# Optimization experiments

Hardware: AMD Instinct MI355X
Metric: run time of the kernel (lower is better)

The kernel has to match this reference:

```python
import math
import jax, jax.numpy as jnp
import numpy as np

HEADS = 8


def setup_inputs() -> dict:
    key = jax.random.key(0)
    ks = jax.random.split(key, 8)
    B, L, S, C = 2, 1024, 2048, 1280
    CORR = 256  # native seg_corr resolution; nearest-upsampled x4 to (1024, 1024)
    sc = 0.02
    return {
        "hidden_states": jax.random.normal(ks[0], (B, L, C), jnp.float32),
        "encoder_hidden_states": jax.random.normal(ks[1], (B, S, C), jnp.float32),
        "seg_corr": jax.random.randint(ks[2], (B, CORR, CORR), 0, 2, jnp.int32),
        "Wq": jax.random.normal(ks[3], (C, C), jnp.float32) * sc,
        "Wk": jax.random.normal(ks[4], (C, C), jnp.float32) * sc,
        "Wv": jax.random.normal(ks[5], (C, C), jnp.float32) * sc,
        "Wo": jax.random.normal(ks[6], (C, C), jnp.float32) * sc,
        "bo": jnp.zeros((C,), jnp.float32),
    }


def reference(hidden_states, encoder_hidden_states, seg_corr, Wq, Wk, Wv, Wo, bo):
    B, L, C = hidden_states.shape
    S = encoder_hidden_states.shape[1]
    H = HEADS
    d = C // H

    # projections -> [B, H, L, d] / [B, H, S, d]
    q = (hidden_states @ Wq).reshape(B, L, H, d).transpose(0, 2, 1, 3)
    k = (encoder_hidden_states @ Wk).reshape(B, S, H, d).transpose(0, 2, 1, 3)
    v = (encoder_hidden_states @ Wv).reshape(B, S, H, d).transpose(0, 2, 1, 3)

    scale = 1.0 / math.sqrt(d)
    scores = jnp.einsum("bhld,bhsd->bhls", q, k) * scale  # [B, H, L, S]

    half = S // 2  # S == 2L in the match-attention branch
    # nearest-neighbor upsample of seg_corr to (L, half) == integer repeat
    rL = L // seg_corr.shape[1]
    rS = half // seg_corr.shape[2]
    corr = jnp.repeat(jnp.repeat(seg_corr, rL, axis=1), rS, axis=2)[:, None]  # [B,1,L,half]

    # hard correlation mask on the second half of keys (reference-image tokens)
    masked = jnp.where(corr == 1, scores[..., half:], jnp.float32(-jnp.inf))
    scores = jnp.concatenate([scores[..., :half], masked], axis=-1)

    attn_weight = jax.nn.softmax(scores, axis=-1)  # dropout_p = 0.0
    out = jnp.einsum("bhls,bhsd->bhld", attn_weight, v)
    out = out.transpose(0, 2, 1, 3).reshape(B, L, C)

    out = out @ Wo + bo            # to_out[0]; to_out[1] dropout is identity at p=0
    out = out + hidden_states      # residual connection; rescale_output_factor = 1
    return out
```

## Files before the change

kernel.cpp:

```cpp
#include <hip/hip_runtime.h>

typedef unsigned short u16;
typedef unsigned int   u32;
typedef unsigned char  u8;

using bf16x8 = __attribute__((ext_vector_type(8))) __bf16;
using f32x4  = __attribute__((ext_vector_type(4))) float;
using s16x4  = __attribute__((ext_vector_type(4))) short;

__device__ __forceinline__ u16 f2bf(float f) {
    u32 u = __float_as_uint(f);
    return (u16)((u + 0x7FFFu + ((u >> 16) & 1u)) >> 16);
}

#define MFMA(a, b, c) __builtin_amdgcn_mfma_f32_16x16x32_bf16((a), (b), (c), 0, 0, 0)
#define MFMA16(a, b, c) __builtin_amdgcn_mfma_f32_16x16x16bf16_1k((a), (b), (c), 0, 0, 0)

__device__ __forceinline__ void gll16(const u16* g, u16* l) {
    __builtin_amdgcn_global_load_lds(
        (const __attribute__((address_space(1))) void*)g,
        (__attribute__((address_space(3))) void*)l, 16, 0, 0);
}

__global__ __launch_bounds__(256) void wtrans_kernel(
    const float* __restrict__ W0, const float* __restrict__ W1,
    const float* __restrict__ W2, const float* __restrict__ W3,
    u16* __restrict__ T0, u16* __restrict__ T1,
    u16* __restrict__ T2, u16* __restrict__ T3) {
    const int N = 1280;
    const int z = blockIdx.z;
    const float* W = (z == 0) ? W0 : (z == 1) ? W1 : (z == 2) ? W2 : W3;
    u16* T = (z == 0) ? T0 : (z == 1) ? T1 : (z == 2) ? T2 : T3;
    __shared__ float t[32][33];
    const int bx = blockIdx.x * 32, by = blockIdx.y * 32;
    const int x = threadIdx.x, ty = threadIdx.y;
#pragma unroll
    for (int j = 0; j < 4; j++) {
        const int y = ty + j * 8;
        t[y][x] = W[(size_t)(by + y) * N + (bx + x)];
    }
    __syncthreads();
#pragma unroll
    for (int j = 0; j < 4; j++) {
        const int y = ty + j * 8;
        T[(size_t)(bx + y) * N + (by + x)] = f2bf(t[x][y]);
    }
}

__global__ __launch_bounds__(256) void conv_kernel(const float* __restrict__ in,
                                                   u16* __restrict__ out, int n8) {
    const int i = blockIdx.x * 256 + threadIdx.x;
    if (i >= n8) return;
    const float4 a = ((const float4*)in)[i * 2];
    const float4 b = ((const float4*)in)[i * 2 + 1];
    union { uint4 u; u16 s[8]; } cv;
    cv.s[0] = f2bf(a.x); cv.s[1] = f2bf(a.y); cv.s[2] = f2bf(a.z); cv.s[3] = f2bf(a.w);
    cv.s[4] = f2bf(b.x); cv.s[5] = f2bf(b.y); cv.s[6] = f2bf(b.z); cv.s[7] = f2bf(b.w);
    ((uint4*)out)[i] = cv.u;
}

template <int MI, bool TRANSC, bool EPI>
__global__ __launch_bounds__(256) void gemm2_kernel(
    const u16* __restrict__ A, const u16* __restrict__ Bt, void* __restrict__ Cp,
    const float* __restrict__ bias, const float* __restrict__ resid,
    const int M, const int N, const int K) {
    __shared__ __align__(16) u16 Al[2][MI * 32 * 64];
    __shared__ __align__(16) u16 Bl[2][128 * 64];
    const int tid = threadIdx.x;
    const int lane = tid & 63, w = tid >> 6;
    const int wr = w >> 1, wc = w & 1;
    const int lr = lane & 15, lq = lane >> 4;
    const int m0 = blockIdx.y * (MI * 32), n0 = blockIdx.x * 128;

    const int f_r = tid >> 3;
    const int srcch = (tid & 7) ^ ((tid >> 3) & 7);
    const int ldst = (tid & 192) * 8;

    const f32x4 fzero = {0.f, 0.f, 0.f, 0.f};
    f32x4 acc[MI][4];
#pragma unroll
    for (int i = 0; i < MI; i++)
#pragma unroll
        for (int j = 0; j < 4; j++) acc[i][j] = fzero;

    const int nkt = K >> 6;

#define STAGE(buf, kt)                                                          \
    {                                                                           \
        const int k0s = (kt) << 6;                                              \
        _Pragma("unroll")                                                       \
        for (int i = 0; i < MI; i++) {                                          \
            const int r = i * 32 + f_r;                                         \
            gll16(&A[(size_t)(m0 + r) * K + k0s + srcch * 8],                   \
                  &Al[buf][i * 2048 + ldst]);                                   \
        }                                                                       \
        _Pragma("unroll")                                                       \
        for (int i = 0; i < 4; i++) {                                           \
            const int r = i * 32 + f_r;                                         \
            gll16(&Bt[(size_t)(n0 + r) * K + k0s + srcch * 8],                  \
                  &Bl[buf][i * 2048 + ldst]);                                   \
        }                                                                       \
    }

    STAGE(0, 0);
    asm volatile("s_waitcnt vmcnt(0)" ::: "memory");
    __syncthreads();
    int cur = 0;
    for (int kt = 0; kt < nkt; kt++) {
        if (kt + 1 < nkt) STAGE(cur ^ 1, kt + 1);
#pragma unroll
        for (int ks = 0; ks < 2; ks++) {
            bf16x8 af[MI], bfv[4];
#pragma unroll
            for (int mi = 0; mi < MI; mi++) {
                const int rowA = wr * (MI * 16) + mi * 16 + lr;
                af[mi] = *(const bf16x8*)&Al[cur][rowA * 64 +
                                                  (((ks * 4 + lq) ^ (rowA & 7)) << 3)];
            }
#pragma unroll
            for (int ni = 0; ni < 4; ni++) {
                const int rowB = wc * 64 + ni * 16 + lr;
                bfv[ni] = *(const bf16x8*)&Bl[cur][rowB * 64 +
                                                   (((ks * 4 + lq) ^ (rowB & 7)) << 3)];
            }
#pragma unroll
            for (int mi = 0; mi < MI; mi++)
#pragma unroll
                for (int ni = 0; ni < 4; ni++)
                    acc[mi][ni] = MFMA(af[mi], bfv[ni], acc[mi][ni]);
        }
        asm volatile("s_waitcnt vmcnt(0)" ::: "memory");
        __syncthreads();
        cur ^= 1;
    }
#undef STAGE

#pragma unroll
    for (int mi = 0; mi < MI; mi++)
#pragma unroll
        for (int ni = 0; ni < 4; ni++)
#pragma unroll
            for (int j = 0; j < 4; j++) {
                const int row = m0 + wr * (MI * 16) + mi * 16 + lq * 4 + j;
                const int col = n0 + wc * 64 + ni * 16 + lr;
                const float v = acc[mi][ni][j];
                if (EPI) {
                    ((float*)Cp)[(size_t)row * N + col] =
                        v + bias[col] + resid[(size_t)row * N + col];
                } else if (TRANSC) {
                    ((u16*)Cp)[((size_t)(col >> 11) * 1280 + row) * 2048 +
                               (col & 2047)] = f2bf(v);
                } else {
                    ((u16*)Cp)[(size_t)row * N + col] = f2bf(v);
                }
            }
}

__global__ __launch_bounds__(256) void attn_kernel(
    const u16* __restrict__ qb, const u16* __restrict__ kb,
    const u16* __restrict__ vtb, const int* __restrict__ seg,
    u16* __restrict__ ao) {
    __shared__ __align__(16) u16 arena[20224];
    const int KL = 0;
    const int VT = 10752;
    const int PT = 17152;
    const int SG = 18944;
    const int ML = 19968;
    u8* segl8 = (u8*)&arena[SG];
    float* Mlf = (float*)&arena[ML];
    float* Osum = (float*)&arena[KL];

    const int tid = threadIdx.x;
    const int lane = tid & 63, w = tid >> 6;
    const int qg = w >> 1, kc = w & 1;
    const int lr = lane & 15, lq = lane >> 4;
    const int id = blockIdx.x;
    const int h = id & 7, bz = (id >> 3) & 1, qt = id >> 4;

#pragma unroll
    for (int i = 0; i < 2; i++) {
        const int4 v =
            *(const int4*)&seg[(size_t)(bz * 256 + qt * 8) * 256 + tid * 8 + i * 4];
        segl8[tid * 8 + i * 4 + 0] = (u8)v.x;
        segl8[tid * 8 + i * 4 + 1] = (u8)v.y;
        segl8[tid * 8 + i * 4 + 2] = (u8)v.z;
        segl8[tid * 8 + i * 4 + 3] = (u8)v.w;
    }

    bf16x8 qf[5];
    {
        const size_t qrow =
            (size_t)(bz * 1024 + qt * 32 + qg * 16 + lr) * 1280 + h * 160;
#pragma unroll
        for (int ks = 0; ks < 5; ks++)
            qf[ks] = *(const bf16x8*)&qb[qrow + ks * 32 + lq * 8];
    }

    const int nk0 = tid, nk1 = tid + 256;
    const int nv0 = tid, nv1 = tid + 256;
    const bool exK = (tid < 128);
    const int ne = exK ? (512 + tid) : (512 + tid - 128);
    const int gok0 = (nk0 / 20) * 1280 + (nk0 % 20) * 8;
    const int lok0 = (nk0 / 20) * 168 + (nk0 % 20) * 8;
    const int gok1 = (nk1 / 20) * 1280 + (nk1 % 20) * 8;
    const int lok1 = (nk1 / 20) * 168 + (nk1 % 20) * 8;
    const int gov0 = (nv0 >> 2) * 2048 + (nv0 & 3) * 8;
    const int lov0 = (nv0 >> 2) * 40 + (nv0 & 3) * 8;
    const int gov1 = (nv1 >> 2) * 2048 + (nv1 & 3) * 8;
    const int lov1 = (nv1 >> 2) * 40 + (nv1 & 3) * 8;
    const int goe = exK ? ((ne / 20) * 1280 + (ne % 20) * 8)
                        : ((ne >> 2) * 2048 + (ne & 3) * 8);
    const int loe = exK ? ((ne / 20) * 168 + (ne % 20) * 8)
                        : ((ne >> 2) * 40 + (ne & 3) * 8);

    const u16* kT = kb + (size_t)(bz * 2048) * 1280 + h * 160;
    const u16* vT = vtb + (size_t)(bz * 1280 + h * 160) * 2048;

    const f32x4 fzero = {0.f, 0.f, 0.f, 0.f};
    f32x4 oacc[10];
#pragma unroll
    for (int d = 0; d < 10; d++) oacc[d] = fzero;
    f32x4 oaccL = fzero;
    float m_i[4] = {0.f, 0.f, 0.f, 0.f};
    const float sc = 0.07905694150420949f;
    const s16x4 ones = {(short)0x3F80, (short)0x3F80, (short)0x3F80, (short)0x3F80};
    u16* ptw = &arena[PT + w * 448];

    uint4 rk0 = *(const uint4*)&kT[gok0];
    uint4 rk1 = *(const uint4*)&kT[gok1];
    uint4 rv0 = *(const uint4*)&vT[gov0];
    uint4 rv1 = *(const uint4*)&vT[gov1];
    uint4 re  = exK ? *(const uint4*)&kT[goe] : *(const uint4*)&vT[goe];

    for (int kt = 0; kt < 64; kt++) {
        __syncthreads();
        *(uint4*)&arena[KL + lok0] = rk0;
        *(uint4*)&arena[KL + lok1] = rk1;
        *(uint4*)&arena[VT + lov0] = rv0;
        *(uint4*)&arena[VT + lov1] = rv1;
        if (exK) *(uint4*)&arena[KL + loe] = re;
        else     *(uint4*)&arena[VT + loe] = re;
        if (kt + 1 < 64) {
            const u16* kTn = kT + (size_t)(kt + 1) * 40960;
            const u16* vTn = vT + (kt + 1) * 32;
            rk0 = *(const uint4*)&kTn[gok0];
            rk1 = *(const uint4*)&kTn[gok1];
            rv0 = *(const uint4*)&vTn[gov0];
            rv1 = *(const uint4*)&vTn[gov1];
            re  = exK ? *(const uint4*)&kTn[goe] : *(const uint4*)&vTn[goe];
        }
        __syncthreads();

        f32x4 s4 = fzero;
#pragma unroll
        for (int ks = 0; ks < 5; ks++) {
            const bf16x8 bk =
                *(const bf16x8*)&arena[KL + (kc * 16 + lr) * 168 + ks * 32 + lq * 8];
            s4 = MFMA(qf[ks], bk, s4);
        }
        float msk = 0.f;
        if (kt >= 32) {
            const int sg = (kt - 32) * 8 + kc * 4 + (lr >> 2);
            msk = segl8[(qg * 4 + lq) * 256 + sg] ? 0.f : -1e30f;
        }
#pragma unroll
        for (int j = 0; j < 4; j++) s4[j] = s4[j] * sc + msk;

        const bool ex = (s4[0] > m_i[0] + 8.f) || (s4[1] > m_i[1] + 8.f) ||
                        (s4[2] > m_i[2] + 8.f) || (s4[3] > m_i[3] + 8.f);
        if (__any(ex)) {
#pragma unroll
            for (int j = 0; j < 4; j++) {
                float rm = s4[j];
                rm = fmaxf(rm, __shfl_xor(rm, 1));
                rm = fmaxf(rm, __shfl_xor(rm, 2));
                rm = fmaxf(rm, __shfl_xor(rm, 4));
                rm = fmaxf(rm, __shfl_xor(rm, 8));
                const float mn = fmaxf(m_i[j], rm);
                const float al = __expf(m_i[j] - mn);
#pragma unroll
                for (int d = 0; d < 10; d++) oacc[d][j] *= al;
                oaccL[j] *= al;
                m_i[j] = mn;
            }
        }
#pragma unroll
        for (int j = 0; j < 4; j++) {
            const float e = __expf(s4[j] - m_i[j]);
            ptw[(lq * 4 + j) * 28 + lr] = f2bf(e);
        }
        const s16x4 pa = *(const s16x4*)&ptw[lr * 28 + lq * 4];
        oaccL = MFMA16(pa, ones, oaccL);
#pragma unroll
        for (int nt2 = 0; nt2 < 10; nt2++) {
            const s16x4 bv =
                *(const s16x4*)&arena[VT + (nt2 * 16 + lr) * 40 + kc * 16 + lq * 4];
            oacc[nt2] = MFMA16(pa, bv, oacc[nt2]);
        }
    }

    if (lr == 0) {
#pragma unroll
        for (int j = 0; j < 4; j++) {
            Mlf[(w * 16 + lq * 4 + j) * 2 + 0] = m_i[j];
            Mlf[(w * 16 + lq * 4 + j) * 2 + 1] = oaccL[j];
        }
    }
    __syncthreads();
    float aj[4], inv[4];
#pragma unroll
    for (int j = 0; j < 4; j++) {
        const int row = lq * 4 + j;
        const float m1 = Mlf[((w ^ 1) * 16 + row) * 2];
        const float l1 = Mlf[((w ^ 1) * 16 + row) * 2 + 1];
        const float M = fmaxf(m_i[j], m1);
        aj[j] = __expf(m_i[j] - M);
        inv[j] = 1.f / (oaccL[j] * aj[j] + l1 * __expf(m1 - M));
    }
    if (kc == 1) {
#pragma unroll
        for (int nt2 = 0; nt2 < 10; nt2++)
#pragma unroll
            for (int j = 0; j < 4; j++)
                Osum[(qg * 16 + lq * 4 + j) * 164 + nt2 * 16 + lr] =
                    oacc[nt2][j] * aj[j];
    }
    __syncthreads();
    if (kc == 0) {
#pragma unroll
        for (int nt2 = 0; nt2 < 10; nt2++)
#pragma unroll
            for (int j = 0; j < 4; j++) {
                const int row = lq * 4 + j;
                const float v = (oacc[nt2][j] * aj[j] +
                                 Osum[(qg * 16 + row) * 164 + nt2 * 16 + lr]) *
                                inv[j];
                ao[(size_t)(bz * 1024 + qt * 32 + qg * 16 + row) * 1280 + h * 160 +
                   nt2 * 16 + lr] = f2bf(v);
            }
    }
}

extern "C" void kernel_launch(void* const* d_in, const int* in_sizes, int n_in,
                              void* d_out, int out_size, void* d_ws, size_t ws_size,
                              hipStream_t stream) {
    const float* hs  = (const float*)d_in[0];
    const float* ehs = (const float*)d_in[1];
    const int*   seg = (const int*)d_in[2];
    const float* Wq  = (const float*)d_in[3];
    const float* Wk  = (const float*)d_in[4];
    const float* Wv  = (const float*)d_in[5];
    const float* Wo  = (const float*)d_in[6];
    const float* bo  = (const float*)d_in[7];
    float* out = (float*)d_out;

    u16* base  = (u16*)d_ws;
    u16* WoT   = base;
    u16* qbuf  = WoT + 1638400;
    u16* kbuf  = qbuf + 2621440;
    u16* vtbuf = kbuf + 5242880;
    u16* hbuf  = vtbuf + 5242880;
    u16* ebuf  = hbuf + 2621440;
    u16* WqT   = ebuf + 5242880;
    u16* WkT   = WqT + 1638400;
    u16* WvT   = WkT + 1638400;
    u16* aobuf = hbuf;

    dim3 tb(32, 8), tg(40, 40, 4);
    wtrans_kernel<<<tg, tb, 0, stream>>>(Wq, Wk, Wv, Wo, WqT, WkT, WvT, WoT);
    conv_kernel<<<1280, 256, 0, stream>>>(hs, hbuf, 327680);
    conv_kernel<<<2560, 256, 0, stream>>>(ehs, ebuf, 655360);

    gemm2_kernel<2, false, false><<<dim3(10, 32), 256, 0, stream>>>(
        hbuf, WqT, qbuf, nullptr, nullptr, 2048, 1280, 1280);
    gemm2_kernel<4, false, false><<<dim3(10, 32), 256, 0, stream>>>(
        ebuf, WkT, kbuf, nullptr, nullptr, 4096, 1280, 1280);
    gemm2_kernel<4, true, false><<<dim3(32, 10), 256, 0, stream>>>(
        WvT, ebuf, vtbuf, nullptr, nullptr, 1280, 4096, 1280);

    attn_kernel<<<512, 256, 0, stream>>>(qbuf, kbuf, vtbuf, seg, aobuf);

    gemm2_kernel<2, false, true><<<dim3(10, 32), 256, 0, stream>>>(
        aobuf, WoT, out, bo, hs, 2048, 1280, 1280);
}
```

Baseline: 190.8 us.

## Double attention key tile, use 16x16x32 MFMA for PV, shrink GEMM tiles

The attention kernel now processes 64 keys per iteration instead of 32, halving loop trips and barriers. Each wave computes two 16-key score tiles and uses the wider 16x16x32 bf16 MFMA for both P·V and the row-sum, with K/V staged through more LDS per iteration. Separately, the projection GEMMs switch to smaller M tiles, doubling grid size so more CUs stay busy, and the two fp32-to-bf16 conversion launches merge into one. The larger LDS footprint and register use may reduce attention occupancy, and the smaller GEMM tiles reduce data reuse per block.

```diff
diff --git a/kernel.cpp b/kernel.cpp
--- a/kernel.cpp
+++ b/kernel.cpp
@@ -6,7 +6,6 @@
 
 using bf16x8 = __attribute__((ext_vector_type(8))) __bf16;
 using f32x4  = __attribute__((ext_vector_type(4))) float;
-using s16x4  = __attribute__((ext_vector_type(4))) short;
 
 __device__ __forceinline__ u16 f2bf(float f) {
     u32 u = __float_as_uint(f);
@@ -14,7 +13,6 @@
 }
 
 #define MFMA(a, b, c) __builtin_amdgcn_mfma_f32_16x16x32_bf16((a), (b), (c), 0, 0, 0)
-#define MFMA16(a, b, c) __builtin_amdgcn_mfma_f32_16x16x16bf16_1k((a), (b), (c), 0, 0, 0)
 
 __device__ __forceinline__ void gll16(const u16* g, u16* l) {
     __builtin_amdgcn_global_load_lds(
@@ -47,10 +45,14 @@
     }
 }
 
-__global__ __launch_bounds__(256) void conv_kernel(const float* __restrict__ in,
-                                                   u16* __restrict__ out, int n8) {
-    const int i = blockIdx.x * 256 + threadIdx.x;
-    if (i >= n8) return;
+__global__ __launch_bounds__(256) void conv2_kernel(const float* __restrict__ in0,
+                                                    u16* __restrict__ out0,
+                                                    const float* __restrict__ in1,
+                                                    u16* __restrict__ out1) {
+    const int bid = blockIdx.x;
+    const float* in = (bid < 1280) ? in0 : in1;
+    u16* out = (bid < 1280) ? out0 : out1;
+    const int i = ((bid < 1280) ? bid : bid - 1280) * 256 + threadIdx.x;
     const float4 a = ((const float4*)in)[i * 2];
     const float4 b = ((const float4*)in)[i * 2 + 1];
     union { uint4 u; u16 s[8]; } cv;
@@ -160,12 +162,12 @@
     const u16* __restrict__ qb, const u16* __restrict__ kb,
     const u16* __restrict__ vtb, const int* __restrict__ seg,
     u16* __restrict__ ao) {
-    __shared__ __align__(16) u16 arena[20224];
+    __shared__ __align__(16) u16 arena[26112];
     const int KL = 0;
     const int VT = 10752;
-    const int PT = 17152;
-    const int SG = 18944;
-    const int ML = 19968;
+    const int PT = 22272;
+    const int SG = 24832;
+    const int ML = 25856;
     u8* segl8 = (u8*)&arena[SG];
     float* Mlf = (float*)&arena[ML];
     float* Osum = (float*)&arena[KL];
@@ -196,25 +198,20 @@
             qf[ks] = *(const bf16x8*)&qb[qrow + ks * 32 + lq * 8];
     }
 
-    const int nk0 = tid, nk1 = tid + 256;
-    const int nv0 = tid, nv1 = tid + 256;
-    const bool exK = (tid < 128);
-    const int ne = exK ? (512 + tid) : (512 + tid - 128);
-    const int gok0 = (nk0 / 20) * 1280 + (nk0 % 20) * 8;
-    const int lok0 = (nk0 / 20) * 168 + (nk0 % 20) * 8;
-    const int gok1 = (nk1 / 20) * 1280 + (nk1 % 20) * 8;
-    const int lok1 = (nk1 / 20) * 168 + (nk1 % 20) * 8;
-    const int gov0 = (nv0 >> 2) * 2048 + (nv0 & 3) * 8;
-    const int lov0 = (nv0 >> 2) * 40 + (nv0 & 3) * 8;
-    const int gov1 = (nv1 >> 2) * 2048 + (nv1 & 3) * 8;
-    const int lov1 = (nv1 >> 2) * 40 + (nv1 & 3) * 8;
-    const int goe = exK ? ((ne / 20) * 1280 + (ne % 20) * 8)
-                        : ((ne >> 2) * 2048 + (ne & 3) * 8);
-    const int loe = exK ? ((ne / 20) * 168 + (ne % 20) * 8)
-                        : ((ne >> 2) * 40 + (ne & 3) * 8);
-
-    const u16* kT = kb + (size_t)(bz * 2048) * 1280 + h * 160;
-    const u16* vT = vtb + (size_t)(bz * 1280 + h * 160) * 2048;
+    int gok[5], lok[5], gov[5], lov[5];
+#pragma unroll
+    for (int i = 0; i < 5; i++) {
+        const int n = i * 256 + tid;
+        const int kr = n / 20, kcol = n % 20;
+        gok[i] = kr * 1280 + kcol * 8;
+        lok[i] = kr * 168 + kcol * 8;
+        const int d = n >> 3, vc = n & 7;
+        gov[i] = d * 2048 + vc * 8;
+        lov[i] = d * 72 + vc * 8;
+    }
+
+    const u16* kP = kb + (size_t)(bz * 2048) * 1280 + h * 160;
+    const u16* vP = vtb + (size_t)(bz * 1280 + h * 160) * 2048;
 
     const f32x4 fzero = {0.f, 0.f, 0.f, 0.f};
     f32x4 oacc[10];
@@ -223,55 +220,69 @@
     f32x4 oaccL = fzero;
     float m_i[4] = {0.f, 0.f, 0.f, 0.f};
     const float sc = 0.07905694150420949f;
-    const s16x4 ones = {(short)0x3F80, (short)0x3F80, (short)0x3F80, (short)0x3F80};
-    u16* ptw = &arena[PT + w * 448];
-
-    uint4 rk0 = *(const uint4*)&kT[gok0];
-    uint4 rk1 = *(const uint4*)&kT[gok1];
-    uint4 rv0 = *(const uint4*)&vT[gov0];
-    uint4 rv1 = *(const uint4*)&vT[gov1];
-    uint4 re  = exK ? *(const uint4*)&kT[goe] : *(const uint4*)&vT[goe];
-
-    for (int kt = 0; kt < 64; kt++) {
+    bf16x8 ones8;
+#pragma unroll
+    for (int e = 0; e < 8; e++) {
+        const u16 one = 0x3F80;
+        ones8[e] = *(const __bf16*)&one;
+    }
+    u16* ptw = &arena[PT + w * 640];
+
+    uint4 rk[5], rv[5];
+#pragma unroll
+    for (int i = 0; i < 5; i++) {
+        rk[i] = *(const uint4*)&kP[gok[i]];
+        rv[i] = *(const uint4*)&vP[gov[i]];
+    }
+
+    for (int kt = 0; kt < 32; kt++) {
         __syncthreads();
-        *(uint4*)&arena[KL + lok0] = rk0;
-        *(uint4*)&arena[KL + lok1] = rk1;
-        *(uint4*)&arena[VT + lov0] = rv0;
-        *(uint4*)&arena[VT + lov1] = rv1;
-        if (exK) *(uint4*)&arena[KL + loe] = re;
-        else     *(uint4*)&arena[VT + loe] = re;
-        if (kt + 1 < 64) {
-            const u16* kTn = kT + (size_t)(kt + 1) * 40960;
-            const u16* vTn = vT + (kt + 1) * 32;
-            rk0 = *(const uint4*)&kTn[gok0];
-            rk1 = *(const uint4*)&kTn[gok1];
-            rv0 = *(const uint4*)&vTn[gov0];
-            rv1 = *(const uint4*)&vTn[gov1];
-            re  = exK ? *(const uint4*)&kTn[goe] : *(const uint4*)&vTn[goe];
+#pragma unroll
+        for (int i = 0; i < 5; i++) {
+            *(uint4*)&arena[KL + lok[i]] = rk[i];
+            *(uint4*)&arena[VT + lov[i]] = rv[i];
+        }
+        kP += 81920;
+        vP += 64;
+        if (kt + 1 < 32) {
+#pragma unroll
+            for (int i = 0; i < 5; i++) {
+                rk[i] = *(const uint4*)&kP[gok[i]];
+                rv[i] = *(const uint4*)&vP[gov[i]];
+            }
         }
         __syncthreads();
 
-        f32x4 s4 = fzero;
-#pragma unroll
-        for (int ks = 0; ks < 5; ks++) {
-            const bf16x8 bk =
-                *(const bf16x8*)&arena[KL + (kc * 16 + lr) * 168 + ks * 32 + lq * 8];
-            s4 = MFMA(qf[ks], bk, s4);
-        }
-        float msk = 0.f;
-        if (kt >= 32) {
-            const int sg = (kt - 32) * 8 + kc * 4 + (lr >> 2);
-            msk = segl8[(qg * 4 + lq) * 256 + sg] ? 0.f : -1e30f;
-        }
-#pragma unroll
-        for (int j = 0; j < 4; j++) s4[j] = s4[j] * sc + msk;
-
-        const bool ex = (s4[0] > m_i[0] + 8.f) || (s4[1] > m_i[1] + 8.f) ||
-                        (s4[2] > m_i[2] + 8.f) || (s4[3] > m_i[3] + 8.f);
+        f32x4 s[2] = {fzero, fzero};
+#pragma unroll
+        for (int ks = 0; ks < 5; ks++)
+#pragma unroll
+            for (int nt = 0; nt < 2; nt++) {
+                const bf16x8 bk = *(const bf16x8*)
+                    &arena[KL + (kc * 32 + nt * 16 + lr) * 168 + ks * 32 + lq * 8];
+                s[nt] = MFMA(qf[ks], bk, s[nt]);
+            }
+
+#pragma unroll
+        for (int nt = 0; nt < 2; nt++) {
+            float msk = 0.f;
+            if (kt >= 16) {
+                const int sg = (kt - 16) * 16 + kc * 8 + nt * 4 + (lr >> 2);
+                msk = segl8[(qg * 4 + lq) * 256 + sg] ? 0.f : -1e30f;
+            }
+#pragma unroll
+            for (int j = 0; j < 4; j++) s[nt][j] = s[nt][j] * sc + msk;
+        }
+
+        bool ex = false;
+#pragma unroll
+        for (int nt = 0; nt < 2; nt++)
+#pragma unroll
+            for (int j = 0; j < 4; j++) ex |= (s[nt][j] > m_i[j] + 8.f);
         if (__any(ex)) {
 #pragma unroll
             for (int j = 0; j < 4; j++) {
-                float rm = s4[j];
+                float rm = fmaxf(s[0][j], s[1][j]);
                 rm = fmaxf(rm, __shfl_xor(rm, 1));
                 rm = fmaxf(rm, __shfl_xor(rm, 2));
                 rm = fmaxf(rm, __shfl_xor(rm, 4));
@@ -285,17 +296,20 @@
             }
         }
 #pragma unroll
-        for (int j = 0; j < 4; j++) {
-            const float e = __expf(s4[j] - m_i[j]);
-            ptw[(lq * 4 + j) * 28 + lr] = f2bf(e);
-        }
-        const s16x4 pa = *(const s16x4*)&ptw[lr * 28 + lq * 4];
-        oaccL = MFMA16(pa, ones, oaccL);
+        for (int nt = 0; nt < 2; nt++)
+#pragma unroll
+            for (int j = 0; j < 4; j++) {
+                const float e = __expf(s[nt][j] - m_i[j]);
+                *(__bf16*)&ptw[(lq * 4 + j) * 40 + nt * 16 + lr] = (__bf16)e;
+            }
+
+        const bf16x8 pa = *(const bf16x8*)&ptw[lr * 40 + lq * 8];
+        oaccL = MFMA(pa, ones8, oaccL);
 #pragma unroll
         for (int nt2 = 0; nt2 < 10; nt2++) {
-            const s16x4 bv =
-                *(const s16x4*)&arena[VT + (nt2 * 16 + lr) * 40 + kc * 16 + lq * 4];
-            oacc[nt2] = MFMA16(pa, bv, oacc[nt2]);
+            const bf16x8 bv = *(const bf16x8*)
+                &arena[VT + (nt2 * 16 + lr) * 72 + kc * 32 + lq * 8];
+            oacc[nt2] = MFMA(pa, bv, oacc[nt2]);
         }
     }
 
@@ -322,7 +336,7 @@
         for (int nt2 = 0; nt2 < 10; nt2++)
 #pragma unroll
             for (int j = 0; j < 4; j++)
-                Osum[(qg * 16 + lq * 4 + j) * 164 + nt2 * 16 + lr] =
+                Osum[(qg * 16 + lq * 4 + j) * 168 + nt2 * 16 + lr] =
                     oacc[nt2][j] * aj[j];
     }
     __syncthreads();
@@ -333,10 +347,10 @@
             for (int j = 0; j < 4; j++) {
                 const int row = lq * 4 + j;
                 const float v = (oacc[nt2][j] * aj[j] +
-                                 Osum[(qg * 16 + row) * 164 + nt2 * 16 + lr]) *
+                                 Osum[(qg * 16 + row) * 168 + nt2 * 16 + lr]) *
                                 inv[j];
-                ao[(size_t)(bz * 1024 + qt * 32 + qg * 16 + row) * 1280 + h * 160 +
-                   nt2 * 16 + lr] = f2bf(v);
+                *(__bf16*)&ao[(size_t)(bz * 1024 + qt * 32 + qg * 16 + row) * 1280 +
+                              h * 160 + nt2 * 16 + lr] = (__bf16)v;
             }
     }
 }
@@ -368,18 +382,17 @@
 
     dim3 tb(32, 8), tg(40, 40, 4);
     wtrans_kernel<<<tg, tb, 0, stream>>>(Wq, Wk, Wv, Wo, WqT, WkT, WvT, WoT);
-    conv_kernel<<<1280, 256, 0, stream>>>(hs, hbuf, 327680);
-    conv_kernel<<<2560, 256, 0, stream>>>(ehs, ebuf, 655360);
-
-    gemm2_kernel<2, false, false><<<dim3(10, 32), 256, 0, stream>>>(
+    conv2_kernel<<<3840, 256, 0, stream>>>(hs, hbuf, ehs, ebuf);
+
+    gemm2_kernel<1, false, false><<<dim3(10, 64), 256, 0, stream>>>(
         hbuf, WqT, qbuf, nullptr, nullptr, 2048, 1280, 1280);
-    gemm2_kernel<4, false, false><<<dim3(10, 32), 256, 0, stream>>>(
+    gemm2_kernel<2, false, false><<<dim3(10, 64), 256, 0, stream>>>(
         ebuf, WkT, kbuf, nullptr, nullptr, 4096, 1280, 1280);
-    gemm2_kernel<4, true, false><<<dim3(32, 10), 256, 0, stream>>>(
+    gemm2_kernel<2, true, false><<<dim3(32, 20), 256, 0, stream>>>(
         WvT, ebuf, vtbuf, nullptr, nullptr, 1280, 4096, 1280);
 
     attn_kernel<<<512, 256, 0, stream>>>(qbuf, kbuf, vtbuf, seg, aobuf);
 
-    gemm2_kernel<2, false, true><<<dim3(10, 32), 256, 0, stream>>>(
+    gemm2_kernel<1, false, true><<<dim3(10, 64), 256, 0, stream>>>(
         aobuf, WoT, out, bo, hs, 2048, 1280, 1280);
 }
```

New measurement: 292.4 us. 1.53x slower.
